# Kernel tuning notes

Hardware: AMD Instinct MI355X
Metric: run time of the kernel (lower is better)

Reference implementation:

```python
import jax, jax.numpy as jnp
import numpy as np

NHEAD = 16

def setup_inputs() -> dict:
    key = jax.random.key(0)
    ks = jax.random.split(key, 7)
    B, S, D = 4, 2048, 1024
    enc = jax.random.normal(ks[0], (B, S, D), dtype=jnp.float32)
    padMask = jax.random.randint(ks[1], (B, S), 0, 2) == 1  # True = padded
    w = 0.02
    Wq = jax.random.normal(ks[2], (D, D), dtype=jnp.float32) * w
    Wk = jax.random.normal(ks[3], (D, D), dtype=jnp.float32) * w
    Wv = jax.random.normal(ks[4], (D, D), dtype=jnp.float32) * w
    Wo = jax.random.normal(ks[5], (D, D), dtype=jnp.float32) * w
    z = jnp.zeros((D,), dtype=jnp.float32)
    return {"encodedSeq": enc, "padMask": padMask,
            "Wq": Wq, "bq": z, "Wk": Wk, "bk": z,
            "Wv": Wv, "bv": z, "Wo": Wo, "bo": z}


def _split(x, nhead):
    B, S, D = x.shape
    return x.reshape(B, S, nhead, D // nhead).transpose(0, 2, 1, 3)  # [B,H,S,Dh]


def reference(encodedSeq, padMask, Wq, bq, Wk, bk, Wv, bv, Wo, bo):
    B, S, D = encodedSeq.shape
    H = NHEAD
    Dh = D // H
    # torch Linear: y = x @ W.T + b
    Q = _split(encodedSeq @ Wq.T + bq, H)
    K = _split(encodedSeq @ Wk.T + bk, H)
    V = _split(encodedSeq @ Wv.T + bv, H)
    # NOTE: original divides by head_dim (encDim // nhead), not sqrt(head_dim)
    scores = jnp.einsum('bhsd,bhtd->bhst', Q, K) / Dh  # [B,H,S,S]
    # masked_fill on both padded query rows and padded key cols with -1e8
    mask = padMask[:, None, :, None] | padMask[:, None, None, :]
    scores = jnp.where(mask, jnp.float32(-1e8), scores)
    attn = jax.nn.softmax(scores, axis=-1)
    attnV = jnp.einsum('bhst,bhtd->bhsd', attn, V)
    concat = attnV.transpose(0, 2, 1, 3).reshape(B, S, D)
    return concat @ Wo.T + bo
```

## Files before the change

### kernel.cpp

```cpp
#include <hip/hip_runtime.h>
#include <hip/hip_bf16.h>


#define SS 2048
#define DD 1024

typedef __attribute__((ext_vector_type(8))) short short8;
typedef __attribute__((ext_vector_type(8))) __bf16 bfv8;
typedef __attribute__((ext_vector_type(4))) float f32x4;
typedef __attribute__((ext_vector_type(4))) unsigned u32x4;

__device__ __forceinline__ unsigned short f2bf(float x) {
  unsigned u = __builtin_bit_cast(unsigned, x);
  u += 0x7fffu + ((u >> 16) & 1u);
  return (unsigned short)(u >> 16);
}

__device__ __forceinline__ unsigned cvtpk_bf16(float lo, float hi) {
  unsigned r;
  asm("v_cvt_pk_bf16_f32 %0, %1, %2" : "=v"(r) : "v"(lo), "v"(hi));
  return r;
}

__device__ __forceinline__ void gload_lds16(const void* gsrc, void* ldst) {
  __builtin_amdgcn_global_load_lds(
      (const __attribute__((address_space(1))) unsigned int*)(unsigned long long)gsrc,
      (__attribute__((address_space(3))) unsigned int*)(unsigned int)(unsigned long long)ldst,
      16, 0, 0);
}

template <typename V>
__device__ __forceinline__ auto mfma_sel(V a, V b, f32x4 c, int)
    -> decltype(__builtin_amdgcn_mfma_f32_16x16x32_bf16(a, b, c, 0, 0, 0)) {
  return __builtin_amdgcn_mfma_f32_16x16x32_bf16(a, b, c, 0, 0, 0);
}
template <typename V>
__device__ __forceinline__ f32x4 mfma_sel(V a, V b, f32x4 c, long) {
  return __builtin_amdgcn_mfma_f32_16x16x32_bf16(
      __builtin_bit_cast(bfv8, a), __builtin_bit_cast(bfv8, b), c, 0, 0, 0);
}
__device__ __forceinline__ f32x4 MFMA(short8 a, short8 b, f32x4 c) {
  return mfma_sel(a, b, c, 0);
}

__global__ __launch_bounds__(256) void cvt_f32_bf16(
    const float* __restrict__ src, unsigned short* __restrict__ dst, int n8) {
  int i = blockIdx.x * blockDim.x + threadIdx.x;
  if (i < n8) {
    float4 a = ((const float4*)src)[2 * i];
    float4 b = ((const float4*)src)[2 * i + 1];
    short8 o;
    o[0] = f2bf(a.x); o[1] = f2bf(a.y); o[2] = f2bf(a.z); o[3] = f2bf(a.w);
    o[4] = f2bf(b.x); o[5] = f2bf(b.y); o[6] = f2bf(b.z); o[7] = f2bf(b.w);
    ((short8*)dst)[i] = o;
  }
}

__global__ __launch_bounds__(256) void cvt_w4(
    const float* __restrict__ w0, const float* __restrict__ w1,
    const float* __restrict__ w2, const float* __restrict__ w3,
    unsigned short* __restrict__ o0, unsigned short* __restrict__ o1,
    unsigned short* __restrict__ o2, unsigned short* __restrict__ o3) {
  const float* s; unsigned short* d;
  switch (blockIdx.y) {
    case 0: s = w0; d = o0; break;
    case 1: s = w1; d = o1; break;
    case 2: s = w2; d = o2; break;
    default: s = w3; d = o3; break;
  }
  int i = blockIdx.x * blockDim.x + threadIdx.x;
  float4 a = ((const float4*)s)[2 * i];
  float4 b = ((const float4*)s)[2 * i + 1];
  short8 o;
  o[0] = f2bf(a.x); o[1] = f2bf(a.y); o[2] = f2bf(a.z); o[3] = f2bf(a.w);
  o[4] = f2bf(b.x); o[5] = f2bf(b.y); o[6] = f2bf(b.z); o[7] = f2bf(b.w);
  ((short8*)d)[i] = o;
}

template <int A_BF16, int W_BF16, int OUT_BF16>
__global__ __launch_bounds__(256) void gemm_bt(const void* __restrict__ Ain,
                                               const void* __restrict__ Win,
                                               const float* __restrict__ bias,
                                               void* __restrict__ Cout,
                                               float oscale) {
  __shared__ unsigned short As[128 * 32];
  __shared__ unsigned short Bs[128 * 32];
  const int t = threadIdx.x;
  const int lane = t & 63;
  const int w = t >> 6;
  const int l15 = lane & 15, g = lane >> 4;
  const int wr = w >> 1, wc = w & 1;
  const size_t m0 = (size_t)blockIdx.y * 128;
  const int n0 = blockIdx.x * 128;

  f32x4 acc[4][4];
#pragma unroll
  for (int i = 0; i < 4; i++)
#pragma unroll
    for (int j = 0; j < 4; j++) acc[i][j] = {0.f, 0.f, 0.f, 0.f};

  for (int k0 = 0; k0 < DD; k0 += 32) {
    if (A_BF16 && W_BF16) {
      const unsigned short* A = (const unsigned short*)Ain;
      const unsigned short* Wb = (const unsigned short*)Win;
#pragma unroll
      for (int i = 0; i < 2; i++) {
        int blk = i * 4 + w;
        int row = blk * 16 + (lane >> 2);
        int c8 = lane & 3;
        gload_lds16(A + (m0 + row) * DD + k0 + c8 * 8, (char*)As + blk * 1024);
        gload_lds16(Wb + (size_t)(n0 + row) * DD + k0 + c8 * 8,
                    (char*)Bs + blk * 1024);
      }
    } else {
      if (A_BF16) {
        const unsigned short* A = (const unsigned short*)Ain;
#pragma unroll
        for (int i = 0; i < 2; i++) {
          int idx = t + i * 256;
          int row = idx >> 2, c8 = idx & 3;
          *(short8*)(As + row * 32 + c8 * 8) =
              *(const short8*)(A + (m0 + row) * DD + k0 + c8 * 8);
        }
      } else {
        const float* A = (const float*)Ain;
#pragma unroll
        for (int i = 0; i < 4; i++) {
          int idx = t + i * 256;
          int row = idx >> 3, c4 = idx & 7;
          float4 v = *(const float4*)(A + (m0 + row) * DD + k0 + c4 * 4);
          ushort4 o = {f2bf(v.x), f2bf(v.y), f2bf(v.z), f2bf(v.w)};
          *(ushort4*)(As + row * 32 + c4 * 4) = o;
        }
      }
      const float* Wf = (const float*)Win;
#pragma unroll
      for (int i = 0; i < 4; i++) {
        int idx = t + i * 256;
        int row = idx >> 3, c4 = idx & 7;
        float4 v = *(const float4*)(Wf + (size_t)(n0 + row) * DD + k0 + c4 * 4);
        ushort4 o = {f2bf(v.x), f2bf(v.y), f2bf(v.z), f2bf(v.w)};
        *(ushort4*)(Bs + row * 32 + c4 * 4) = o;
      }
    }
    __syncthreads();
    short8 af[4], bfr[4];
#pragma unroll
    for (int mi = 0; mi < 4; mi++)
      af[mi] = *(const short8*)(As + (wr * 64 + mi * 16 + l15) * 32 + g * 8);
#pragma unroll
    for (int ni = 0; ni < 4; ni++)
      bfr[ni] = *(const short8*)(Bs + (wc * 64 + ni * 16 + l15) * 32 + g * 8);
#pragma unroll
    for (int mi = 0; mi < 4; mi++)
#pragma unroll
      for (int ni = 0; ni < 4; ni++)
        acc[mi][ni] = MFMA(af[mi], bfr[ni], acc[mi][ni]);
    __syncthreads();
  }

  float bs[4];
#pragma unroll
  for (int ni = 0; ni < 4; ni++) bs[ni] = bias[n0 + wc * 64 + ni * 16 + l15];
#pragma unroll
  for (int mi = 0; mi < 4; mi++) {
#pragma unroll
    for (int ni = 0; ni < 4; ni++) {
      size_t row = m0 + wr * 64 + mi * 16 + g * 4;
      int col = n0 + wc * 64 + ni * 16 + l15;
#pragma unroll
      for (int j = 0; j < 4; j++) {
        float v = (acc[mi][ni][j] + bs[ni]) * oscale;
        if (OUT_BF16)
          ((unsigned short*)Cout)[(row + j) * DD + col] = f2bf(v);
        else
          ((float*)Cout)[(row + j) * DD + col] = v;
      }
    }
  }
}

__global__ __launch_bounds__(256) void transpose_v(
    const unsigned short* __restrict__ Vb, unsigned short* __restrict__ Vt) {
  __shared__ unsigned short L[64 * 72];
  const int t = threadIdx.x;
  const int s0 = blockIdx.x * 64;
  const int bh = blockIdx.y;
  const int b = bh >> 4, h = bh & 15;
#pragma unroll
  for (int i = 0; i < 2; i++) {
    int idx = t + i * 256;
    int s = idx >> 3, dc = idx & 7;
    *(short8*)(L + s * 72 + dc * 8) =
        *(const short8*)(Vb + ((size_t)b * SS + s0 + s) * DD + h * 64 + dc * 8);
  }
  __syncthreads();
#pragma unroll
  for (int i = 0; i < 2; i++) {
    int idx = t + i * 256;
    int d = idx >> 3, sc = idx & 7;
    short8 o;
#pragma unroll
    for (int e = 0; e < 8; e++) o[e] = (short)L[(sc * 8 + e) * 72 + d];
    *(short8*)(Vt + ((size_t)bh * 64 + d) * SS + s0 + sc * 8) = o;
  }
}

__global__ __launch_bounds__(256) void attn_kernel(
    const unsigned short* __restrict__ Qb, const unsigned short* __restrict__ Kb,
    const unsigned short* __restrict__ Vt, const int* __restrict__ padMask,
    unsigned short* __restrict__ AO) {
  __shared__ unsigned short Ks[64 * 64];
  __shared__ unsigned short Vs[64 * 64];
  __shared__ float KmB[SS];

  const int t = threadIdx.x;
  const int w = t >> 6, lane = t & 63;
  const int c = lane & 15, g = lane >> 4;
  const int a = g >> 1, bsel = g & 1;
  const int bh = blockIdx.y;
  const int b = bh >> 4, h = bh & 15;
  const int q0 = blockIdx.x * 64 + w * 16;
  const size_t baseBS = (size_t)b * SS;

  {
    int4 ma = *(const int4*)(padMask + baseBS + t * 8);
    int4 mb = *(const int4*)(padMask + baseBS + t * 8 + 4);
    float4 fa = {ma.x ? -1e8f : 3e38f, ma.y ? -1e8f : 3e38f,
                 ma.z ? -1e8f : 3e38f, ma.w ? -1e8f : 3e38f};
    float4 fb = {mb.x ? -1e8f : 3e38f, mb.y ? -1e8f : 3e38f,
                 mb.z ? -1e8f : 3e38f, mb.w ? -1e8f : 3e38f};
    *(float4*)(KmB + t * 8) = fa;
    *(float4*)(KmB + t * 8 + 4) = fb;
  }

  short8 aQ[2];
  {
    const unsigned short* qp = Qb + (baseBS + q0 + c) * DD + h * 64 + g * 8;
    aQ[0] = *(const short8*)(qp);
    aQ[1] = *(const short8*)(qp + 32);
  }
  const float qmf = padMask[baseBS + q0 + c] ? -1e8f : 3e38f;

  float m_r = -1e30f, l_r = 0.f;
  f32x4 acc[4];
#pragma unroll
  for (int nb = 0; nb < 4; nb++) acc[nb] = {0.f, 0.f, 0.f, 0.f};

  for (int kt = 0; kt < SS / 64; ++kt) {
    const int kbase = kt * 64;
#pragma unroll
    for (int i = 0; i < 2; i++) {
      int idx = t + i * 256;
      int r = idx >> 3, ch = idx & 7;
      int sw = (ch ^ (r & 7)) * 8;
      *(short8*)(Ks + r * 64 + sw) =
          *(const short8*)(Kb + (baseBS + kbase + r) * DD + h * 64 + ch * 8);
      *(short8*)(Vs + r * 64 + sw) =
          *(const short8*)(Vt + ((size_t)bh * 64 + r) * SS + kbase + ch * 8);
    }
    __syncthreads();

    f32x4 sc[4];
#pragma unroll
    for (int kb = 0; kb < 4; kb++) {
      f32x4 s = {0.f, 0.f, 0.f, 0.f};
#pragma unroll
      for (int kk = 0; kk < 2; kk++) {
        int row = kb * 16 + c;
        short8 ak = *(const short8*)(Ks + row * 64 + ((kk * 4 + g) ^ (c & 7)) * 8);
        s = MFMA(ak, aQ[kk], s);
      }
      sc[kb] = s;
    }

    f32x4 kmf[4];
#pragma unroll
    for (int kb = 0; kb < 4; kb++)
      kmf[kb] = *(const f32x4*)(KmB + kbase + kb * 16 + g * 4);

    float rm = -3e38f;
#pragma unroll
    for (int kb = 0; kb < 4; kb++)
#pragma unroll
      for (int j = 0; j < 4; j++) {
        float sv = fminf(fminf(sc[kb][j], kmf[kb][j]), qmf);
        sc[kb][j] = sv;
        rm = fmaxf(rm, sv);
      }
    rm = fmaxf(rm, __shfl_xor(rm, 16));
    rm = fmaxf(rm, __shfl_xor(rm, 32));

    const bool grow = !__all(rm <= m_r + 8.f);
    const float mnew = grow ? fmaxf(m_r, rm) : m_r;
    float sum = 0.f;
#pragma unroll
    for (int kb = 0; kb < 4; kb++)
#pragma unroll
      for (int j = 0; j < 4; j++) {
        float pv = __expf(sc[kb][j] - mnew);
        sc[kb][j] = pv;
        sum += pv;
      }
    sum += __shfl_xor(sum, 16);
    sum += __shfl_xor(sum, 32);
    if (grow) {
      const float es = __expf(m_r - mnew);
      l_r = l_r * es + sum;
      m_r = mnew;
      float esj[4];
#pragma unroll
      for (int j = 0; j < 4; j++) esj[j] = __shfl(es, 4 * g + j);
#pragma unroll
      for (int nb = 0; nb < 4; nb++)
#pragma unroll
        for (int j = 0; j < 4; j++) acc[nb][j] *= esj[j];
    } else {
      l_r += sum;
    }

    unsigned W0[4], W1[4];
#pragma unroll
    for (int kb = 0; kb < 4; kb++) {
      W0[kb] = cvtpk_bf16(sc[kb][0], sc[kb][1]);
      W1[kb] = cvtpk_bf16(sc[kb][2], sc[kb][3]);
    }
    const int srcA = c + (bsel << 5);
    const int srcB = srcA + 16;
    unsigned A0[4], A1[4], B0[4], B1[4];
#pragma unroll
    for (int f = 0; f < 4; f++) {
      A0[f] = __shfl(W0[f], srcA);
      A1[f] = __shfl(W1[f], srcA);
      B0[f] = __shfl(W0[f], srcB);
      B1[f] = __shfl(W1[f], srcB);
    }
#pragma unroll
    for (int kk = 0; kk < 2; kk++) {
      u32x4 pd;
      pd.x = a ? A0[2 * kk + 1] : A0[2 * kk];
      pd.y = a ? A1[2 * kk + 1] : A1[2 * kk];
      pd.z = a ? B0[2 * kk + 1] : B0[2 * kk];
      pd.w = a ? B1[2 * kk + 1] : B1[2 * kk];
      short8 pa = __builtin_bit_cast(short8, pd);
#pragma unroll
      for (int nb = 0; nb < 4; nb++) {
        int row = nb * 16 + c;
        short8 vb_ = *(const short8*)(Vs + row * 64 + ((kk * 4 + g) ^ (c & 7)) * 8);
        acc[nb] = MFMA(pa, vb_, acc[nb]);
      }
    }
    __syncthreads();
  }

  float lj[4];
#pragma unroll
  for (int j = 0; j < 4; j++) lj[j] = __shfl(l_r, 4 * g + j);
#pragma unroll
  for (int nb = 0; nb < 4; nb++)
#pragma unroll
    for (int j = 0; j < 4; j++) {
      float ov = acc[nb][j] / lj[j];
      AO[(baseBS + q0 + 4 * g + j) * DD + h * 64 + nb * 16 + c] = f2bf(ov);
    }
}

extern "C" void kernel_launch(void* const* d_in, const int* in_sizes, int n_in,
                              void* d_out, int out_size, void* d_ws, size_t ws_size,
                              hipStream_t stream) {
  const float* enc = (const float*)d_in[0];
  const int* padMask = (const int*)d_in[1];
  const float* Wq = (const float*)d_in[2];
  const float* bq = (const float*)d_in[3];
  const float* Wk = (const float*)d_in[4];
  const float* bk = (const float*)d_in[5];
  const float* Wv = (const float*)d_in[6];
  const float* bv = (const float*)d_in[7];
  const float* Wo = (const float*)d_in[8];
  const float* bo = (const float*)d_in[9];
  float* out = (float*)d_out;

  const size_t NTOK = (size_t)4 * SS;
  unsigned short* Qb = (unsigned short*)d_ws;
  unsigned short* Kb = Qb + NTOK * DD;
  unsigned short* Vb = Kb + NTOK * DD;
  unsigned short* Vt = Vb + NTOK * DD;
  unsigned short* AO = Vb;
  unsigned short* Ebf = Vt + NTOK * DD;
  unsigned short* Wqb = Ebf + NTOK * DD;
  unsigned short* Wkb = Wqb + (size_t)DD * DD;
  unsigned short* Wvb = Wkb + (size_t)DD * DD;
  unsigned short* Wob = Wvb + (size_t)DD * DD;

  const size_t need_ext =
      (5 * NTOK * DD + 4 * (size_t)DD * DD) * sizeof(unsigned short);
  const bool ext = ws_size >= need_ext;

  const float QSC = 0.015625f;
  dim3 blk(256);
  dim3 gGemm(DD / 128, NTOK / 128);
  dim3 gT(SS / 64, 4 * 16);

  if (ext) {
    const int n8e = (int)(NTOK * DD / 8);
    const int n8w = DD * DD / 8;
    cvt_f32_bf16<<<n8e / 256, blk, 0, stream>>>(enc, Ebf, n8e);
    cvt_w4<<<dim3(n8w / 256, 4), blk, 0, stream>>>(Wq, Wk, Wv, Wo,
                                                   Wqb, Wkb, Wvb, Wob);
    gemm_bt<1, 1, 1><<<gGemm, blk, 0, stream>>>(Ebf, Wqb, bq, (void*)Qb, QSC);
    gemm_bt<1, 1, 1><<<gGemm, blk, 0, stream>>>(Ebf, Wkb, bk, (void*)Kb, 1.f);
    gemm_bt<1, 1, 1><<<gGemm, blk, 0, stream>>>(Ebf, Wvb, bv, (void*)Vb, 1.f);
    transpose_v<<<gT, blk, 0, stream>>>(Vb, Vt);
    attn_kernel<<<gT, blk, 0, stream>>>(Qb, Kb, Vt, padMask, AO);
    gemm_bt<1, 1, 0><<<gGemm, blk, 0, stream>>>(AO, Wob, bo, (void*)out, 1.f);
  } else {
    gemm_bt<0, 0, 1><<<gGemm, blk, 0, stream>>>(enc, Wq, bq, (void*)Qb, QSC);
    gemm_bt<0, 0, 1><<<gGemm, blk, 0, stream>>>(enc, Wk, bk, (void*)Kb, 1.f);
    gemm_bt<0, 0, 1><<<gGemm, blk, 0, stream>>>(enc, Wv, bv, (void*)Vb, 1.f);
    transpose_v<<<gT, blk, 0, stream>>>(Vb, Vt);
    attn_kernel<<<gT, blk, 0, stream>>>(Qb, Kb, Vt, padMask, AO);
    gemm_bt<1, 0, 0><<<gGemm, blk, 0, stream>>>(AO, Wo, bo, (void*)out, 1.f);
  }
}
```

Before: 379.7 us.

## Fuse QKV GEMMs with XCD-aware swizzle, exp2 softmax, and LDS-staged P in attention

Merges the three Q/K/V projection GEMMs into one launch over the contiguous bf16 weight buffer, using a block-index swizzle that groups M-tiles per XCD for L2 reuse. The output GEMM uses the same swizzled kernel. In attention, log2e is folded into the Q scale so softmax can use the hardware exp2. The P matrix is now staged through a swizzled LDS buffer instead of cross-lane shuffles, with MFMA operands swapped so the output is stored as vectorized rows. This adds LDS traffic and changes mask constants and the rescale threshold, which carries a small numerical risk.

Measured after the change: 326.4 us. -14.0%, faster.

```diff
diff --git a/kernel.cpp b/kernel.cpp
--- a/kernel.cpp
+++ b/kernel.cpp
@@ -4,11 +4,17 @@
 
 #define SS 2048
 #define DD 1024
+#define MM 8192
 
 typedef __attribute__((ext_vector_type(8))) short short8;
 typedef __attribute__((ext_vector_type(8))) __bf16 bfv8;
 typedef __attribute__((ext_vector_type(4))) float f32x4;
 typedef __attribute__((ext_vector_type(4))) unsigned u32x4;
+typedef __attribute__((ext_vector_type(2))) unsigned u32x2;
+typedef __attribute__((ext_vector_type(4))) unsigned short us4;
+
+#define LOG2E 1.4426950408889634f
+#define NEGB (-1.44269504e8f)
 
 __device__ __forceinline__ unsigned short f2bf(float x) {
   unsigned u = __builtin_bit_cast(unsigned, x);
@@ -19,6 +25,12 @@
 __device__ __forceinline__ unsigned cvtpk_bf16(float lo, float hi) {
   unsigned r;
   asm("v_cvt_pk_bf16_f32 %0, %1, %2" : "=v"(r) : "v"(lo), "v"(hi));
+  return r;
+}
+
+__device__ __forceinline__ float exp2_hw(float x) {
+  float r;
+  asm("v_exp_f32 %0, %1" : "=v"(r) : "v"(x));
   return r;
 }
 
@@ -77,9 +89,88 @@
   ((short8*)d)[i] = o;
 }
 
-template <int A_BF16, int W_BF16, int OUT_BF16>
+template <int NMATS, int OUT_BF16>
+__global__ __launch_bounds__(256) void gemm_swz(
+    const unsigned short* __restrict__ A, const unsigned short* __restrict__ Wall,
+    const float* __restrict__ b0, const float* __restrict__ b1,
+    const float* __restrict__ b2, void* __restrict__ Cout,
+    float s0, float s1, float s2) {
+  __shared__ unsigned short As[128 * 32];
+  __shared__ unsigned short Bs[128 * 32];
+  const int bid = blockIdx.x;
+  const int xcd = bid & 7, q = bid >> 3;
+  const int n_blk = q >> 3;
+  const int m_blk = (xcd << 3) + (q & 7);
+  const int mat = (NMATS == 3) ? (n_blk >> 3) : 0;
+  const int n0 = (NMATS == 3) ? ((n_blk & 7) * 128) : (n_blk * 128);
+  const unsigned short* Wb = Wall + (size_t)mat * DD * DD;
+  const float* bias = (mat == 0) ? b0 : (mat == 1 ? b1 : b2);
+  const float osc = (mat == 0) ? s0 : (mat == 1 ? s1 : s2);
+  const size_t m0 = (size_t)m_blk * 128;
+
+  const int t = threadIdx.x;
+  const int lane = t & 63;
+  const int w = t >> 6;
+  const int l15 = lane & 15, g = lane >> 4;
+  const int wr = w >> 1, wc = w & 1;
+
+  f32x4 acc[4][4];
+#pragma unroll
+  for (int i = 0; i < 4; i++)
+#pragma unroll
+    for (int j = 0; j < 4; j++) acc[i][j] = {0.f, 0.f, 0.f, 0.f};
+
+  for (int k0 = 0; k0 < DD; k0 += 32) {
+#pragma unroll
+    for (int i = 0; i < 2; i++) {
+      int blk = i * 4 + w;
+      int row = blk * 16 + (lane >> 2);
+      int c8 = lane & 3;
+      gload_lds16(A + (m0 + row) * DD + k0 + c8 * 8, (char*)As + blk * 1024);
+      gload_lds16(Wb + (size_t)(n0 + row) * DD + k0 + c8 * 8,
+                  (char*)Bs + blk * 1024);
+    }
+    __syncthreads();
+    short8 af[4], bfr[4];
+#pragma unroll
+    for (int mi = 0; mi < 4; mi++)
+      af[mi] = *(const short8*)(As + (wr * 64 + mi * 16 + l15) * 32 + g * 8);
+#pragma unroll
+    for (int ni = 0; ni < 4; ni++)
+      bfr[ni] = *(const short8*)(Bs + (wc * 64 + ni * 16 + l15) * 32 + g * 8);
+#pragma unroll
+    for (int mi = 0; mi < 4; mi++)
+#pragma unroll
+      for (int ni = 0; ni < 4; ni++)
+        acc[mi][ni] = MFMA(af[mi], bfr[ni], acc[mi][ni]);
+    __syncthreads();
+  }
+
+  float bs[4];
+#pragma unroll
+  for (int ni = 0; ni < 4; ni++) bs[ni] = bias[n0 + wc * 64 + ni * 16 + l15];
+#pragma unroll
+  for (int mi = 0; mi < 4; mi++) {
+#pragma unroll
+    for (int ni = 0; ni < 4; ni++) {
+      size_t row = m0 + wr * 64 + mi * 16 + g * 4;
+      int col = n0 + wc * 64 + ni * 16 + l15;
+#pragma unroll
+      for (int j = 0; j < 4; j++) {
+        float v = (acc[mi][ni][j] + bs[ni]) * osc;
+        if (OUT_BF16)
+          ((unsigned short*)Cout + (size_t)mat * MM * DD)[(row + j) * DD + col] =
+              f2bf(v);
+        else
+          ((float*)Cout)[(row + j) * DD + col] = v;
+      }
+    }
+  }
+}
+
+template <int A_BF16, int OUT_BF16>
 __global__ __launch_bounds__(256) void gemm_bt(const void* __restrict__ Ain,
-                                               const void* __restrict__ Win,
+                                               const float* __restrict__ Wf,
                                                const float* __restrict__ bias,
                                                void* __restrict__ Cout,
                                                float oscale) {
@@ -100,48 +191,34 @@
     for (int j = 0; j < 4; j++) acc[i][j] = {0.f, 0.f, 0.f, 0.f};
 
   for (int k0 = 0; k0 < DD; k0 += 32) {
-    if (A_BF16 && W_BF16) {
+    if (A_BF16) {
       const unsigned short* A = (const unsigned short*)Ain;
-      const unsigned short* Wb = (const unsigned short*)Win;
 #pragma unroll
       for (int i = 0; i < 2; i++) {
-        int blk = i * 4 + w;
-        int row = blk * 16 + (lane >> 2);
-        int c8 = lane & 3;
-        gload_lds16(A + (m0 + row) * DD + k0 + c8 * 8, (char*)As + blk * 1024);
-        gload_lds16(Wb + (size_t)(n0 + row) * DD + k0 + c8 * 8,
-                    (char*)Bs + blk * 1024);
+        int idx = t + i * 256;
+        int row = idx >> 2, c8 = idx & 3;
+        *(short8*)(As + row * 32 + c8 * 8) =
+            *(const short8*)(A + (m0 + row) * DD + k0 + c8 * 8);
       }
     } else {
-      if (A_BF16) {
-        const unsigned short* A = (const unsigned short*)Ain;
-#pragma unroll
-        for (int i = 0; i < 2; i++) {
-          int idx = t + i * 256;
-          int row = idx >> 2, c8 = idx & 3;
-          *(short8*)(As + row * 32 + c8 * 8) =
-              *(const short8*)(A + (m0 + row) * DD + k0 + c8 * 8);
-        }
-      } else {
-        const float* A = (const float*)Ain;
-#pragma unroll
-        for (int i = 0; i < 4; i++) {
-          int idx = t + i * 256;
-          int row = idx >> 3, c4 = idx & 7;
-          float4 v = *(const float4*)(A + (m0 + row) * DD + k0 + c4 * 4);
-          ushort4 o = {f2bf(v.x), f2bf(v.y), f2bf(v.z), f2bf(v.w)};
-          *(ushort4*)(As + row * 32 + c4 * 4) = o;
-        }
-      }
-      const float* Wf = (const float*)Win;
+      const float* A = (const float*)Ain;
 #pragma unroll
       for (int i = 0; i < 4; i++) {
         int idx = t + i * 256;
         int row = idx >> 3, c4 = idx & 7;
-        float4 v = *(const float4*)(Wf + (size_t)(n0 + row) * DD + k0 + c4 * 4);
+        float4 v = *(const float4*)(A + (m0 + row) * DD + k0 + c4 * 4);
         ushort4 o = {f2bf(v.x), f2bf(v.y), f2bf(v.z), f2bf(v.w)};
-        *(ushort4*)(Bs + row * 32 + c4 * 4) = o;
-      }
+        *(ushort4*)(As + row * 32 + c4 * 4) = o;
+      }
+    }
+    const float* Wp = Wf;
+#pragma unroll
+    for (int i = 0; i < 4; i++) {
+      int idx = t + i * 256;
+      int row = idx >> 3, c4 = idx & 7;
+      float4 v = *(const float4*)(Wp + (size_t)(n0 + row) * DD + k0 + c4 * 4);
+      ushort4 o = {f2bf(v.x), f2bf(v.y), f2bf(v.z), f2bf(v.w)};
+      *(ushort4*)(Bs + row * 32 + c4 * 4) = o;
     }
     __syncthreads();
     short8 af[4], bfr[4];
@@ -213,11 +290,11 @@
   __shared__ unsigned short Ks[64 * 64];
   __shared__ unsigned short Vs[64 * 64];
   __shared__ float KmB[SS];
+  __shared__ unsigned Ps[4 * 512];
 
   const int t = threadIdx.x;
   const int w = t >> 6, lane = t & 63;
   const int c = lane & 15, g = lane >> 4;
-  const int a = g >> 1, bsel = g & 1;
   const int bh = blockIdx.y;
   const int b = bh >> 4, h = bh & 15;
   const int q0 = blockIdx.x * 64 + w * 16;
@@ -226,10 +303,10 @@
   {
     int4 ma = *(const int4*)(padMask + baseBS + t * 8);
     int4 mb = *(const int4*)(padMask + baseBS + t * 8 + 4);
-    float4 fa = {ma.x ? -1e8f : 3e38f, ma.y ? -1e8f : 3e38f,
-                 ma.z ? -1e8f : 3e38f, ma.w ? -1e8f : 3e38f};
-    float4 fb = {mb.x ? -1e8f : 3e38f, mb.y ? -1e8f : 3e38f,
-                 mb.z ? -1e8f : 3e38f, mb.w ? -1e8f : 3e38f};
+    float4 fa = {ma.x ? NEGB : 3e38f, ma.y ? NEGB : 3e38f,
+                 ma.z ? NEGB : 3e38f, ma.w ? NEGB : 3e38f};
+    float4 fb = {mb.x ? NEGB : 3e38f, mb.y ? NEGB : 3e38f,
+                 mb.z ? NEGB : 3e38f, mb.w ? NEGB : 3e38f};
     *(float4*)(KmB + t * 8) = fa;
     *(float4*)(KmB + t * 8 + 4) = fb;
   }
@@ -240,7 +317,9 @@
     aQ[0] = *(const short8*)(qp);
     aQ[1] = *(const short8*)(qp + 32);
   }
-  const float qmf = padMask[baseBS + q0 + c] ? -1e8f : 3e38f;
+  const float qmf = padMask[baseBS + q0 + c] ? NEGB : 3e38f;
+  const int cx = (c & 7) << 2;
+  unsigned* Pw = Ps + w * 512;
 
   float m_r = -1e30f, l_r = 0.f;
   f32x4 acc[4];
@@ -291,78 +370,61 @@
     rm = fmaxf(rm, __shfl_xor(rm, 16));
     rm = fmaxf(rm, __shfl_xor(rm, 32));
 
-    const bool grow = !__all(rm <= m_r + 8.f);
+    const bool grow = !__all(rm <= m_r + 11.5f);
     const float mnew = grow ? fmaxf(m_r, rm) : m_r;
     float sum = 0.f;
 #pragma unroll
     for (int kb = 0; kb < 4; kb++)
 #pragma unroll
       for (int j = 0; j < 4; j++) {
-        float pv = __expf(sc[kb][j] - mnew);
+        float pv = exp2_hw(sc[kb][j] - mnew);
         sc[kb][j] = pv;
         sum += pv;
       }
     sum += __shfl_xor(sum, 16);
     sum += __shfl_xor(sum, 32);
     if (grow) {
-      const float es = __expf(m_r - mnew);
+      const float es = exp2_hw(m_r - mnew);
       l_r = l_r * es + sum;
       m_r = mnew;
-      float esj[4];
-#pragma unroll
-      for (int j = 0; j < 4; j++) esj[j] = __shfl(es, 4 * g + j);
 #pragma unroll
       for (int nb = 0; nb < 4; nb++)
 #pragma unroll
-        for (int j = 0; j < 4; j++) acc[nb][j] *= esj[j];
+        for (int j = 0; j < 4; j++) acc[nb][j] *= es;
     } else {
       l_r += sum;
     }
 
-    unsigned W0[4], W1[4];
 #pragma unroll
     for (int kb = 0; kb < 4; kb++) {
-      W0[kb] = cvtpk_bf16(sc[kb][0], sc[kb][1]);
-      W1[kb] = cvtpk_bf16(sc[kb][2], sc[kb][3]);
-    }
-    const int srcA = c + (bsel << 5);
-    const int srcB = srcA + 16;
-    unsigned A0[4], A1[4], B0[4], B1[4];
-#pragma unroll
-    for (int f = 0; f < 4; f++) {
-      A0[f] = __shfl(W0[f], srcA);
-      A1[f] = __shfl(W1[f], srcA);
-      B0[f] = __shfl(W0[f], srcB);
-      B1[f] = __shfl(W1[f], srcB);
+      u32x2 pr;
+      pr.x = cvtpk_bf16(sc[kb][0], sc[kb][1]);
+      pr.y = cvtpk_bf16(sc[kb][2], sc[kb][3]);
+      *(u32x2*)(Pw + c * 32 + ((8 * kb + 2 * g) ^ cx)) = pr;
     }
 #pragma unroll
     for (int kk = 0; kk < 2; kk++) {
-      u32x4 pd;
-      pd.x = a ? A0[2 * kk + 1] : A0[2 * kk];
-      pd.y = a ? A1[2 * kk + 1] : A1[2 * kk];
-      pd.z = a ? B0[2 * kk + 1] : B0[2 * kk];
-      pd.w = a ? B1[2 * kk + 1] : B1[2 * kk];
-      short8 pa = __builtin_bit_cast(short8, pd);
+      u32x4 pdw = *(const u32x4*)(Pw + c * 32 + ((16 * kk + 4 * g) ^ cx));
+      short8 pb = __builtin_bit_cast(short8, pdw);
 #pragma unroll
       for (int nb = 0; nb < 4; nb++) {
         int row = nb * 16 + c;
-        short8 vb_ = *(const short8*)(Vs + row * 64 + ((kk * 4 + g) ^ (c & 7)) * 8);
-        acc[nb] = MFMA(pa, vb_, acc[nb]);
-      }
-    }
-    __syncthreads();
-  }
-
-  float lj[4];
-#pragma unroll
-  for (int j = 0; j < 4; j++) lj[j] = __shfl(l_r, 4 * g + j);
-#pragma unroll
-  for (int nb = 0; nb < 4; nb++)
-#pragma unroll
-    for (int j = 0; j < 4; j++) {
-      float ov = acc[nb][j] / lj[j];
-      AO[(baseBS + q0 + 4 * g + j) * DD + h * 64 + nb * 16 + c] = f2bf(ov);
-    }
+        short8 va = *(const short8*)(Vs + row * 64 + ((kk * 4 + g) ^ (c & 7)) * 8);
+        acc[nb] = MFMA(va, pb, acc[nb]);
+      }
+    }
+    __syncthreads();
+  }
+
+  const float inv = 1.f / l_r;
+  const size_t orow = (baseBS + q0 + c) * DD + h * 64;
+#pragma unroll
+  for (int nb = 0; nb < 4; nb++) {
+    us4 o;
+#pragma unroll
+    for (int j = 0; j < 4; j++) o[j] = f2bf(acc[nb][j] * inv);
+    *(us4*)(AO + orow + nb * 16 + 4 * g) = o;
+  }
 }
 
 extern "C" void kernel_launch(void* const* d_in, const int* in_sizes, int n_in,
@@ -380,7 +442,7 @@
   const float* bo = (const float*)d_in[9];
   float* out = (float*)d_out;
 
-  const size_t NTOK = (size_t)4 * SS;
+  const size_t NTOK = (size_t)MM;
   unsigned short* Qb = (unsigned short*)d_ws;
   unsigned short* Kb = Qb + NTOK * DD;
   unsigned short* Vb = Kb + NTOK * DD;
@@ -396,9 +458,8 @@
       (5 * NTOK * DD + 4 * (size_t)DD * DD) * sizeof(unsigned short);
   const bool ext = ws_size >= need_ext;
 
-  const float QSC = 0.015625f;
+  const float QSC = LOG2E / 64.f;
   dim3 blk(256);
-  dim3 gGemm(DD / 128, NTOK / 128);
   dim3 gT(SS / 64, 4 * 16);
 
   if (ext) {
@@ -407,18 +468,19 @@
     cvt_f32_bf16<<<n8e / 256, blk, 0, stream>>>(enc, Ebf, n8e);
     cvt_w4<<<dim3(n8w / 256, 4), blk, 0, stream>>>(Wq, Wk, Wv, Wo,
                                                    Wqb, Wkb, Wvb, Wob);
-    gemm_bt<1, 1, 1><<<gGemm, blk, 0, stream>>>(Ebf, Wqb, bq, (void*)Qb, QSC);
-    gemm_bt<1, 1, 1><<<gGemm, blk, 0, stream>>>(Ebf, Wkb, bk, (void*)Kb, 1.f);
-    gemm_bt<1, 1, 1><<<gGemm, blk, 0, stream>>>(Ebf, Wvb, bv, (void*)Vb, 1.f);
+    gemm_swz<3, 1><<<1536, blk, 0, stream>>>(Ebf, Wqb, bq, bk, bv, (void*)Qb,
+                                             QSC, 1.f, 1.f);
     transpose_v<<<gT, blk, 0, stream>>>(Vb, Vt);
     attn_kernel<<<gT, blk, 0, stream>>>(Qb, Kb, Vt, padMask, AO);
-    gemm_bt<1, 1, 0><<<gGemm, blk, 0, stream>>>(AO, Wob, bo, (void*)out, 1.f);
+    gemm_swz<1, 0><<<512, blk, 0, stream>>>(AO, Wob, bo, bo, bo, (void*)out,
+                                            1.f, 1.f, 1.f);
   } else {
-    gemm_bt<0, 0, 1><<<gGemm, blk, 0, stream>>>(enc, Wq, bq, (void*)Qb, QSC);
-    gemm_bt<0, 0, 1><<<gGemm, blk, 0, stream>>>(enc, Wk, bk, (void*)Kb, 1.f);
-    gemm_bt<0, 0, 1><<<gGemm, blk, 0, stream>>>(enc, Wv, bv, (void*)Vb, 1.f);
+    dim3 gGemm(DD / 128, NTOK / 128);
+    gemm_bt<0, 1><<<gGemm, blk, 0, stream>>>(enc, Wq, bq, (void*)Qb, QSC);
+    gemm_bt<0, 1><<<gGemm, blk, 0, stream>>>(enc, Wk, bk, (void*)Kb, 1.f);
+    gemm_bt<0, 1><<<gGemm, blk, 0, stream>>>(enc, Wv, bv, (void*)Vb, 1.f);
     transpose_v<<<gT, blk, 0, stream>>>(Vb, Vt);
     attn_kernel<<<gT, blk, 0, stream>>>(Qb, Kb, Vt, padMask, AO);
-    gemm_bt<1, 0, 0><<<gGemm, blk, 0, stream>>>(AO, Wo, bo, (void*)out, 1.f);
-  }
-}
+    gemm_bt<1, 0><<<gGemm, blk, 0, stream>>>(AO, Wo, bo, (void*)out, 1.f);
+  }
+}
```
